# Kernel tuning notes

Hardware: AMD Instinct MI355X
Metric: run time of the kernel (lower is better)

## Reference

```python
import jax, jax.numpy as jnp
import numpy as np

B, T, I, H, V = 128, 80, 4096, 256, 6000
DEC_STEPS = 40


def _lstm_cell(x, h, c, Wih, Whh, b):
    # PyTorch gate order: i, f, g, o
    gates = x @ Wih.T + h @ Whh.T + b  # (B, 4H)
    i, f, g, o = jnp.split(gates, 4, axis=-1)
    c_new = jax.nn.sigmoid(f) * c + jax.nn.sigmoid(i) * jnp.tanh(g)
    h_new = jax.nn.sigmoid(o) * jnp.tanh(c_new)
    return h_new, c_new


def _lstm_scan(xs, h0, c0, Wih, Whh, b):
    # xs: (T, B, D)
    def step(carry, x):
        h, c = carry
        h, c = _lstm_cell(x, h, c, Wih, Whh, b)
        return (h, c), h
    (h, c), ys = jax.lax.scan(step, (h0, c0), xs)
    return ys, h, c


def setup_inputs() -> dict:
    key = jax.random.key(0)
    ks = jax.random.split(key, 11)
    s = 1.0 / np.sqrt(H)  # pytorch default LSTM init scale
    return {
        "x": jax.random.normal(ks[0], (B, T, I), jnp.float32),
        "W_ih1": jax.random.uniform(ks[1], (4 * H, I), jnp.float32, -s, s),
        "W_hh1": jax.random.uniform(ks[2], (4 * H, H), jnp.float32, -s, s),
        "b_ih1": jax.random.uniform(ks[3], (4 * H,), jnp.float32, -s, s),
        "b_hh1": jax.random.uniform(ks[4], (4 * H,), jnp.float32, -s, s),
        "W_ih2": jax.random.uniform(ks[5], (4 * H, H), jnp.float32, -s, s),
        "W_hh2": jax.random.uniform(ks[6], (4 * H, H), jnp.float32, -s, s),
        "b_ih2": jax.random.uniform(ks[7], (4 * H,), jnp.float32, -s, s),
        "b_ih2": jax.random.uniform(ks[7], (4 * H,), jnp.float32, -s, s),
        "b_hh2": jax.random.uniform(ks[8], (4 * H,), jnp.float32, -s, s),
        "W_out": jax.random.uniform(ks[9], (V, H), jnp.float32, -s, s),
        "b_out": jax.random.uniform(ks[10], (V,), jnp.float32, -s, s),
    }


def reference(x, W_ih1, W_hh1, b_ih1, b_hh1, W_ih2, W_hh2, b_ih2, b_hh2, W_out, b_out):
    batch = x.shape[0]
    b1 = b_ih1 + b_hh1
    b2 = b_ih2 + b_hh2
    z = jnp.zeros((batch, H), x.dtype)

    # --- Encoding: lstm1 over video features, lstm2 over lstm1 outputs ---
    xs = jnp.transpose(x, (1, 0, 2))  # (T, B, I)
    ys1, h1, c1 = _lstm_scan(xs, z, z, W_ih1, W_hh1, b1)
    _, h2, c2 = _lstm_scan(ys1, z, z, W_ih2, W_hh2, b2)

    # --- One extra lstm1 step with zero padding (as in the source) ---
    dec_pad = jnp.zeros((batch, I), x.dtype)
    h1, c1 = _lstm_cell(dec_pad, h1, c1, W_ih1, W_hh1, b1)
    y2 = jnp.zeros((batch, H), x.dtype)

    def dec_step(carry, _):
        h1, c1, h2, c2, y2 = carry
        h1, c1 = _lstm_cell(dec_pad, h1, c1, W_ih1, W_hh1, b1)
        h2, c2 = _lstm_cell(h1 + y2, h2, c2, W_ih2, W_hh2, b2)
        return (h1, c1, h2, c2, h2), h2

    _, ys = jax.lax.scan(dec_step, (h1, c1, h2, c2, y2), None, length=DEC_STEPS)  # (40, B, H)
    feats = jnp.transpose(ys, (1, 0, 2)).reshape(-1, H)  # (B*40, H)
    return feats @ W_out.T + b_out  # (B*40, V)
```

## Files before the change

### kernel.cpp

```cpp
#include <hip/hip_runtime.h>

#define NB 128
#define NT 80
#define NI 4096
#define NH 256
#define G4 1024
#define NV 6000
#define NVP 6016
#define NDEC 40

typedef unsigned short ushort_t;
typedef __attribute__((ext_vector_type(8))) short bf16x8;
typedef __attribute__((ext_vector_type(4))) float f32x4;

__device__ __forceinline__ unsigned short f2bf(float f) {
  unsigned int x = __float_as_uint(f);
  x += 0x7FFFu + ((x >> 16) & 1u);
  return (unsigned short)(x >> 16);
}
__device__ __forceinline__ float bf2f(ushort_t u) {
  return __uint_as_float(((unsigned)u) << 16);
}
__device__ __forceinline__ ushort4 pack4(float4 v) {
  return make_ushort4(f2bf(v.x), f2bf(v.y), f2bf(v.z), f2bf(v.w));
}
__device__ __forceinline__ float ftanh(float x) {
  float xc = fminf(fmaxf(x, -12.f), 12.f);
  float e = __expf(2.f * xc);
  return (e - 1.f) * __builtin_amdgcn_rcpf(e + 1.f);
}
__device__ __forceinline__ float fsig(float x) {
  return __builtin_amdgcn_rcpf(1.f + __expf(-x));
}


__global__ __launch_bounds__(256) void k_cast_x(const float* __restrict__ x,
                                                ushort_t* __restrict__ xb) {
  const int t = blockIdx.x, b = blockIdx.y;
  const float* src = x + ((size_t)b * NT + t) * NI;
  ushort_t* dst = xb + ((size_t)t * NB + b) * NI;
#pragma unroll
  for (int s = 0; s < 4; ++s) {
    int j = s * 1024 + threadIdx.x * 4;
    float4 v = *(const float4*)(src + j);
    *(ushort4*)(dst + j) = pack4(v);
  }
}

__global__ __launch_bounds__(256) void k_cast_pad(const float* __restrict__ s,
                                                  ushort_t* __restrict__ d,
                                                  int nsrc, int ndst) {
  int i = (blockIdx.x * 256 + threadIdx.x) * 4;
  if (i >= ndst) return;
  ushort4 o;
  if (i < nsrc) {
    float4 v = *(const float4*)(s + i);
    o = pack4(v);
  } else {
    o = make_ushort4(0, 0, 0, 0);
  }
  *(ushort4*)(d + i) = o;
}

__global__ __launch_bounds__(256) void k_addw_bf(const float* __restrict__ a,
                                                 const float* __restrict__ b,
                                                 ushort_t* __restrict__ o) {
  int i = (blockIdx.x * 256 + threadIdx.x) * 4;
  float4 va = *(const float4*)(a + i);
  float4 vb = *(const float4*)(b + i);
  va.x += vb.x; va.y += vb.y; va.z += vb.z; va.w += vb.w;
  *(ushort4*)(o + i) = pack4(va);
}

__global__ __launch_bounds__(256) void k_subh(ushort_t* __restrict__ H1,
                                              const ushort_t* __restrict__ h2) {
  int i = (blockIdx.x * 256 + threadIdx.x) * 4;
  ushort_t* p = H1 + (size_t)NB * NH + i;
  const ushort_t* q = h2 + i;
#pragma unroll
  for (int k = 0; k < 4; ++k) p[k] = f2bf(bf2f(p[k]) - bf2f(q[k]));
}


#define GLDS(gp, lp)                                                     \
  __builtin_amdgcn_global_load_lds(                                      \
      (const __attribute__((address_space(1))) unsigned int*)(gp),       \
      (__attribute__((address_space(3))) unsigned int*)(lp), 16, 0, 0)

__global__ __launch_bounds__(256) void k_gemm(
    const ushort_t* __restrict__ A, const ushort_t* __restrict__ Bm,
    float* __restrict__ C, const float* __restrict__ ba,
    const float* __restrict__ bb, int Nreal, int K, int ldc, int mtiles) {
  __shared__ __align__(16) ushort_t Als[128 * 32];
  __shared__ __align__(16) ushort_t Bls[128 * 32];
  const int bid = blockIdx.x;
  const int mt = bid % mtiles, nt = bid / mtiles;
  const size_t m0 = (size_t)mt * 128, n0 = (size_t)nt * 128;
  const int tid = threadIdx.x, wave = tid >> 6, lane = tid & 63;
  const int wm = (wave & 1) * 64, wn = (wave >> 1) * 64;
  const int srow = wave * 16 + (lane >> 2), skcol = (lane & 3) * 8;
  const int fr = lane & 15, kb = (lane >> 4) * 8;

  f32x4 acc[4][4];
#pragma unroll
  for (int i = 0; i < 4; ++i)
#pragma unroll
    for (int j = 0; j < 4; ++j) acc[i][j] = (f32x4){0.f, 0.f, 0.f, 0.f};

  for (int kk = 0; kk < K; kk += 32) {
    __syncthreads();
#pragma unroll
    for (int p = 0; p < 2; ++p) {
      GLDS(A + (m0 + p * 64 + srow) * K + kk + skcol,
           &Als[(p * 64 + wave * 16) * 32]);
      GLDS(Bm + (n0 + p * 64 + srow) * K + kk + skcol,
           &Bls[(p * 64 + wave * 16) * 32]);
    }
    __syncthreads();
    bf16x8 af[4], bfr[4];
#pragma unroll
    for (int i = 0; i < 4; ++i)
      af[i] = *(const bf16x8*)&Als[(wm + i * 16 + fr) * 32 + kb];
#pragma unroll
    for (int j = 0; j < 4; ++j)
      bfr[j] = *(const bf16x8*)&Bls[(wn + j * 16 + fr) * 32 + kb];
#pragma unroll
    for (int i = 0; i < 4; ++i)
#pragma unroll
      for (int j = 0; j < 4; ++j)
        acc[i][j] = __builtin_amdgcn_mfma_f32_16x16x32_bf16(af[i], bfr[j],
                                                            acc[i][j], 0, 0, 0);
  }
  const int cr4 = (lane >> 4) * 4, ccn = lane & 15;
#pragma unroll
  for (int j = 0; j < 4; ++j) {
    int n = (int)n0 + wn + j * 16 + ccn;
    if (n < Nreal) {
      float bv = (ba ? ba[n] : 0.f) + (bb ? bb[n] : 0.f);
#pragma unroll
      for (int i = 0; i < 4; ++i) {
#pragma unroll
        for (int r = 0; r < 4; ++r) {
          size_t m = m0 + wm + i * 16 + cr4 + r;
          C[m * (size_t)ldc + n] = acc[i][j][r] + bv;
        }
      }
    }
  }
}


struct ChainArgs {
  const float* gIn0; const float* gIn1; int n0; int tStart; int tEnd;
  const ushort_t* W0;
  const float* biasA; const float* biasB;
  ushort_t* traj0; ushort_t* traj1; int t1bmaj;
  ushort_t* hSt; float* cSt;
};

#define LOAD_WREGS(Wb)                                                        \
  _Pragma("unroll") for (int g = 0; g < 3; ++g)                               \
  _Pragma("unroll") for (int h = 0; h < 2; ++h)                               \
  _Pragma("unroll") for (int kb = 0; kb < 8; ++kb)                            \
      wr[g * 2 + h][kb] = *(const bf16x8*)((Wb) +                             \
          (size_t)(g * 256 + cbase + h * 16 + cn) * NH + kb * 32 + kgrp * 8);

#define PIN_W()                                                               \
  _Pragma("unroll") for (int g = 0; g < 6; ++g)                               \
  _Pragma("unroll") for (int kb = 0; kb < 8; ++kb)                            \
      asm volatile("" : "+a"(wr[g][kb]));

#define LOAD_WLDS(Wb)                                                         \
  _Pragma("unroll") for (int h = 0; h < 2; ++h)                               \
  _Pragma("unroll") for (int kb = 0; kb < 8; ++kb)                            \
      *(bf16x8*)&WL[wv * 8192 + h * 4096 + kb * 512 + cn * 32 + kgrp * 8] =   \
          *(const bf16x8*)((Wb) +                                             \
          (size_t)(768 + cbase + h * 16 + cn) * NH + kb * 32 + kgrp * 8);

__device__ __forceinline__ void run_chain(const ChainArgs a, int bg,
                                          ushort_t* WL,
                                          ushort_t (*hTz)[16 * 264]) {
  const int tid = threadIdx.x;
  const int wv = tid >> 6, lane = tid & 63;
  const int cn = lane & 15;
  const int kgrp = lane >> 4;
  const int cbase = wv * 32;
  const int rsel = kgrp & 1;

  bf16x8 wr[6][8];
  LOAD_WREGS(a.W0);
  PIN_W();
  LOAD_WLDS(a.W0);

  for (int i = tid; i < 2 * 16 * 264; i += 512) ((ushort_t*)hTz)[i] = 0;
  __syncthreads();
  float cs[8];
  if (a.tStart == 0) {
#pragma unroll
    for (int i = 0; i < 8; ++i) cs[i] = 0.f;
  } else {
    for (int i = tid; i < 8 * 256; i += 512) {
      int b = i >> 8, col = i & 255;
      hTz[0][b * 264 + col] = a.hSt[(size_t)(bg * 8 + b) * NH + col];
    }
#pragma unroll
    for (int h = 0; h < 2; ++h)
#pragma unroll
      for (int e = 0; e < 4; ++e)
        cs[h * 4 + e] =
            a.cSt[(size_t)(bg * 8 + rsel * 4 + e) * NH + cbase + h * 16 + cn];
  }
  __syncthreads();

  int cur = 0;
  for (int t = a.tStart; t < a.tEnd; ++t) {
    const ushort_t* hTc = &hTz[cur][0];
    ushort_t* hTn = &hTz[cur ^ 1][0];
    const float* gseg = (t < a.n0) ? a.gIn0 : a.gIn1;
    const int tt = (t < a.n0) ? t : t - a.n0;
#pragma unroll
    for (int h = 0; h < 2; ++h) {
      const int gcol = cbase + h * 16 + cn;
      float in_[4][4];
      if (gseg) {
        const float* base = gseg + (size_t)tt * (NB * G4);
#pragma unroll
        for (int g = 0; g < 4; ++g)
#pragma unroll
          for (int e = 0; e < 4; ++e)
            in_[g][e] = base[(size_t)(bg * 8 + rsel * 4 + e) * G4 + g * 256 + gcol];
      } else {
#pragma unroll
        for (int g = 0; g < 4; ++g) {
          float b = a.biasA[g * 256 + gcol] + a.biasB[g * 256 + gcol];
#pragma unroll
          for (int e = 0; e < 4; ++e) in_[g][e] = b;
        }
      }
      f32x4 acc[4];
#pragma unroll
      for (int g = 0; g < 4; ++g) acc[g] = (f32x4){0.f, 0.f, 0.f, 0.f};
#pragma unroll
      for (int kb = 0; kb < 8; ++kb) {
        bf16x8 af = *(const bf16x8*)&hTc[cn * 264 + kb * 32 + kgrp * 8];
        bf16x8 bo = *(const bf16x8*)&WL[wv * 8192 + h * 4096 + kb * 512 +
                                        cn * 32 + kgrp * 8];
        acc[0] = __builtin_amdgcn_mfma_f32_16x16x32_bf16(af, wr[0 + h][kb],
                                                         acc[0], 0, 0, 0);
        acc[1] = __builtin_amdgcn_mfma_f32_16x16x32_bf16(af, wr[2 + h][kb],
                                                         acc[1], 0, 0, 0);
        acc[2] = __builtin_amdgcn_mfma_f32_16x16x32_bf16(af, wr[4 + h][kb],
                                                         acc[2], 0, 0, 0);
        acc[3] = __builtin_amdgcn_mfma_f32_16x16x32_bf16(af, bo, acc[3], 0, 0, 0);
      }
#pragma unroll
      for (int e = 0; e < 4; ++e) {
        float a0 = acc[0][e] + in_[0][e];
        float a1 = acc[1][e] + in_[1][e];
        float a2 = acc[2][e] + in_[2][e];
        float a3 = acc[3][e] + in_[3][e];
        float ig = fsig(a0);
        float fg = fsig(a1);
        float gg = ftanh(a2);
        float og = fsig(a3);
        float cn_ = fg * cs[h * 4 + e] + ig * gg;
        cs[h * 4 + e] = cn_;
        float hn = og * ftanh(cn_);
        unsigned short hb = f2bf(hn);
        if (lane < 32) {
          const int b = (lane >> 4) * 4 + e;
          hTn[b * 264 + gcol] = hb;
          const int bglob = bg * 8 + b;
          if (t < a.n0) {
            if (a.traj0)
              a.traj0[(size_t)t * (NB * NH) + (size_t)bglob * NH + gcol] = hb;
          } else if (a.traj1) {
            size_t idx = a.t1bmaj
                ? ((size_t)bglob * NDEC + (t - a.n0)) * NH + gcol
                : (size_t)(t - a.n0) * (NB * NH) + (size_t)bglob * NH + gcol;
            a.traj1[idx] = hb;
          }
        }
      }
    }
    __syncthreads();
    cur ^= 1;
  }

  for (int i = tid; i < 8 * 256; i += 512) {
    int b = i >> 8, col = i & 255;
    a.hSt[(size_t)(bg * 8 + b) * NH + col] = hTz[cur][b * 264 + col];
  }
  if (lane < 32) {
#pragma unroll
    for (int h = 0; h < 2; ++h)
#pragma unroll
      for (int e = 0; e < 4; ++e)
        a.cSt[(size_t)(bg * 8 + (lane >> 4) * 4 + e) * NH + cbase + h * 16 + cn] =
            cs[h * 4 + e];
  }
}

__global__ __launch_bounds__(512, 1) void p_lstm16(ChainArgs a) {
  __shared__ __align__(16) ushort_t WL[8 * 8192];
  __shared__ __align__(16) ushort_t hTz[2][16 * 264];
  run_chain(a, blockIdx.x, WL, hTz);
}

__global__ __launch_bounds__(512, 1) void p_dual(ChainArgs a, ChainArgs b) {
  __shared__ __align__(16) ushort_t WL[8 * 8192];
  __shared__ __align__(16) ushort_t hTz[2][16 * 264];
  if (blockIdx.x < 16)
    run_chain(a, blockIdx.x, WL, hTz);
  else
    run_chain(b, blockIdx.x - 16, WL, hTz);
}


extern "C" void kernel_launch(void* const* d_in, const int* in_sizes, int n_in,
                              void* d_out, int out_size, void* d_ws,
                              size_t ws_size, hipStream_t stream) {
  const float* x = (const float*)d_in[0];
  const float* Wih1 = (const float*)d_in[1];
  const float* Whh1 = (const float*)d_in[2];
  const float* bih1 = (const float*)d_in[3];
  const float* bhh1 = (const float*)d_in[4];
  const float* Wih2 = (const float*)d_in[5];
  const float* Whh2 = (const float*)d_in[6];
  const float* bih2 = (const float*)d_in[7];
  const float* bhh2 = (const float*)d_in[8];
  const float* Wout = (const float*)d_in[9];
  const float* bout = (const float*)d_in[10];
  char* ws = (char*)d_ws;

  ushort_t* x_bf   = (ushort_t*)(ws + 0);
  float*    G2buf  = (float*)(ws + 0);
  float*    G3buf  = (float*)(ws + 41943040);
  float*    Gbuf   = (float*)(ws + 83886080);
  ushort_t* Wih1b  = (ushort_t*)(ws + 125829120);
  ushort_t* Wih2b  = (ushort_t*)(ws + 134217728);
  ushort_t* Woutb  = (ushort_t*)(ws + 134742016);
  ushort_t* Whh1b  = (ushort_t*)(ws + 137822208);
  ushort_t* Whh2b  = (ushort_t*)(ws + 138346496);
  ushort_t* ys1    = (ushort_t*)(ws + 138870784);
  ushort_t* H1dec  = (ushort_t*)(ws + 144113664);
  ushort_t* feats  = (ushort_t*)(ws + 146800640);
  ushort_t* Wsumb  = (ushort_t*)(ws + 149422080);
  ushort_t* h1St   = (ushort_t*)(ws + 149946368);
  float*    c1St   = (float*)(ws + 150011904);
  ushort_t* h2St   = (ushort_t*)(ws + 150142976);
  float*    c2St   = (float*)(ws + 150208512);

  k_cast_x<<<dim3(NT, NB), 256, 0, stream>>>(x, x_bf);
  k_cast_pad<<<4096, 256, 0, stream>>>(Wih1, Wih1b, G4 * NI, G4 * NI);
  k_cast_pad<<<256, 256, 0, stream>>>(Wih2, Wih2b, G4 * NH, G4 * NH);
  k_cast_pad<<<1504, 256, 0, stream>>>(Wout, Woutb, NV * NH, NVP * NH);
  k_cast_pad<<<256, 256, 0, stream>>>(Whh1, Whh1b, G4 * NH, G4 * NH);
  k_cast_pad<<<256, 256, 0, stream>>>(Whh2, Whh2b, G4 * NH, G4 * NH);
  k_addw_bf<<<256, 256, 0, stream>>>(Wih2, Whh2, Wsumb);

  k_gemm<<<640, 256, 0, stream>>>(x_bf, Wih1b, Gbuf, bih1, bhh1, G4, NI, G4, 80);

  ChainArgs c1{Gbuf, nullptr, NT, 0, 0, Whh1b,
               bih1, bhh1, ys1, H1dec, 0, h1St, c1St};
  ChainArgs c2{G2buf, G3buf, NT, 0, 0, Whh2b,
               bih2, bhh2, nullptr, feats, 1, h2St, c2St};

  ChainArgs e1a = c1; e1a.tStart = 0; e1a.tEnd = 40;
  p_lstm16<<<16, 512, 0, stream>>>(e1a);

  k_gemm<<<320, 256, 0, stream>>>(ys1, Wih2b, G2buf, bih2, bhh2, G4, NH, G4, 40);

  ChainArgs e1b = c1; e1b.tStart = 40; e1b.tEnd = 80;
  ChainArgs e2a = c2; e2a.tStart = 0; e2a.tEnd = 40;
  p_dual<<<32, 512, 0, stream>>>(e1b, e2a);

  k_gemm<<<320, 256, 0, stream>>>(ys1 + (size_t)40 * NB * NH, Wih2b,
                                  G2buf + (size_t)40 * NB * G4, bih2, bhh2,
                                  G4, NH, G4, 40);

  ChainArgs p1 = c1; p1.tStart = 80; p1.tEnd = 121;
  ChainArgs e2b = c2; e2b.tStart = 40; e2b.tEnd = 80;
  p_dual<<<32, 512, 0, stream>>>(p1, e2b);

  k_subh<<<32, 256, 0, stream>>>(H1dec, h2St);

  k_gemm<<<320, 256, 0, stream>>>(H1dec + (size_t)NB * NH, Wih2b, G3buf, bih2,
                                  bhh2, G4, NH, G4, 40);

  ChainArgs d2 = c2; d2.W0 = Wsumb; d2.tStart = 80; d2.tEnd = 120;
  p_lstm16<<<16, 512, 0, stream>>>(d2);

  k_gemm<<<40 * 47, 256, 0, stream>>>(feats, Woutb, (float*)d_out, bout, nullptr,
                                      NV, NH, NV, 40);
}
```

Before: 1.184 ms.

## Double recurrent LSTM block width to 16 waves, one column tile per wave

The recurrent LSTM kernels now launch 1024 threads (16 waves) per block instead of 512. Each wave owns 16 hidden columns instead of 32, which halves the register-resident recurrent weights per wave and drops the inner h loop. The h-state A fragments are also preloaded into registers before the MFMA loop. The aim is to shorten each serial timestep by spreading the per-step matmul and gate math over more waves, at the cost of a heavier block-wide barrier each step and the same 16-block grid.

```diff
diff --git a/kernel.cpp b/kernel.cpp
--- a/kernel.cpp
+++ b/kernel.cpp
@@ -160,22 +160,20 @@
 
 #define LOAD_WREGS(Wb)                                                        \
   _Pragma("unroll") for (int g = 0; g < 3; ++g)                               \
-  _Pragma("unroll") for (int h = 0; h < 2; ++h)                               \
   _Pragma("unroll") for (int kb = 0; kb < 8; ++kb)                            \
-      wr[g * 2 + h][kb] = *(const bf16x8*)((Wb) +                             \
-          (size_t)(g * 256 + cbase + h * 16 + cn) * NH + kb * 32 + kgrp * 8);
+      wr[g][kb] = *(const bf16x8*)((Wb) +                                     \
+          (size_t)(g * 256 + cbase + cn) * NH + kb * 32 + kgrp * 8);
 
 #define PIN_W()                                                               \
-  _Pragma("unroll") for (int g = 0; g < 6; ++g)                               \
+  _Pragma("unroll") for (int g = 0; g < 3; ++g)                               \
   _Pragma("unroll") for (int kb = 0; kb < 8; ++kb)                            \
       asm volatile("" : "+a"(wr[g][kb]));
 
 #define LOAD_WLDS(Wb)                                                         \
-  _Pragma("unroll") for (int h = 0; h < 2; ++h)                               \
   _Pragma("unroll") for (int kb = 0; kb < 8; ++kb)                            \
-      *(bf16x8*)&WL[wv * 8192 + h * 4096 + kb * 512 + cn * 32 + kgrp * 8] =   \
+      *(bf16x8*)&WL[wv * 4096 + kb * 512 + cn * 32 + kgrp * 8] =              \
           *(const bf16x8*)((Wb) +                                             \
-          (size_t)(768 + cbase + h * 16 + cn) * NH + kb * 32 + kgrp * 8);
+          (size_t)(768 + cbase + cn) * NH + kb * 32 + kgrp * 8);
 
 __device__ __forceinline__ void run_chain(const ChainArgs a, int bg,
                                           ushort_t* WL,
@@ -184,31 +182,28 @@
   const int wv = tid >> 6, lane = tid & 63;
   const int cn = lane & 15;
   const int kgrp = lane >> 4;
-  const int cbase = wv * 32;
+  const int cbase = wv * 16;
   const int rsel = kgrp & 1;
 
-  bf16x8 wr[6][8];
+  bf16x8 wr[3][8];
   LOAD_WREGS(a.W0);
   PIN_W();
   LOAD_WLDS(a.W0);
 
-  for (int i = tid; i < 2 * 16 * 264; i += 512) ((ushort_t*)hTz)[i] = 0;
+  for (int i = tid; i < 2 * 16 * 264; i += 1024) ((ushort_t*)hTz)[i] = 0;
   __syncthreads();
-  float cs[8];
+  float cs[4];
   if (a.tStart == 0) {
 #pragma unroll
-    for (int i = 0; i < 8; ++i) cs[i] = 0.f;
+    for (int i = 0; i < 4; ++i) cs[i] = 0.f;
   } else {
-    for (int i = tid; i < 8 * 256; i += 512) {
+    for (int i = tid; i < 8 * 256; i += 1024) {
       int b = i >> 8, col = i & 255;
       hTz[0][b * 264 + col] = a.hSt[(size_t)(bg * 8 + b) * NH + col];
     }
 #pragma unroll
-    for (int h = 0; h < 2; ++h)
-#pragma unroll
-      for (int e = 0; e < 4; ++e)
-        cs[h * 4 + e] =
-            a.cSt[(size_t)(bg * 8 + rsel * 4 + e) * NH + cbase + h * 16 + cn];
+    for (int e = 0; e < 4; ++e)
+      cs[e] = a.cSt[(size_t)(bg * 8 + rsel * 4 + e) * NH + cbase + cn];
   }
   __syncthreads();
 
@@ -218,97 +213,95 @@
     ushort_t* hTn = &hTz[cur ^ 1][0];
     const float* gseg = (t < a.n0) ? a.gIn0 : a.gIn1;
     const int tt = (t < a.n0) ? t : t - a.n0;
-#pragma unroll
-    for (int h = 0; h < 2; ++h) {
-      const int gcol = cbase + h * 16 + cn;
-      float in_[4][4];
-      if (gseg) {
-        const float* base = gseg + (size_t)tt * (NB * G4);
-#pragma unroll
-        for (int g = 0; g < 4; ++g)
-#pragma unroll
-          for (int e = 0; e < 4; ++e)
-            in_[g][e] = base[(size_t)(bg * 8 + rsel * 4 + e) * G4 + g * 256 + gcol];
-      } else {
-#pragma unroll
-        for (int g = 0; g < 4; ++g) {
-          float b = a.biasA[g * 256 + gcol] + a.biasB[g * 256 + gcol];
-#pragma unroll
-          for (int e = 0; e < 4; ++e) in_[g][e] = b;
+    const int gcol = cbase + cn;
+
+    float in_[4][4];
+    if (gseg) {
+      const float* base = gseg + (size_t)tt * (NB * G4);
+#pragma unroll
+      for (int g = 0; g < 4; ++g)
+#pragma unroll
+        for (int e = 0; e < 4; ++e)
+          in_[g][e] = base[(size_t)(bg * 8 + rsel * 4 + e) * G4 + g * 256 + gcol];
+    } else {
+#pragma unroll
+      for (int g = 0; g < 4; ++g) {
+        float b = a.biasA[g * 256 + gcol] + a.biasB[g * 256 + gcol];
+#pragma unroll
+        for (int e = 0; e < 4; ++e) in_[g][e] = b;
+      }
+    }
+    bf16x8 af[8];
+#pragma unroll
+    for (int kb = 0; kb < 8; ++kb)
+      af[kb] = *(const bf16x8*)&hTc[cn * 264 + kb * 32 + kgrp * 8];
+    f32x4 acc[4];
+#pragma unroll
+    for (int g = 0; g < 4; ++g) acc[g] = (f32x4){0.f, 0.f, 0.f, 0.f};
+#pragma unroll
+    for (int kb = 0; kb < 8; ++kb) {
+      bf16x8 bo = *(const bf16x8*)&WL[wv * 4096 + kb * 512 + cn * 32 + kgrp * 8];
+      acc[0] = __builtin_amdgcn_mfma_f32_16x16x32_bf16(af[kb], wr[0][kb],
+                                                       acc[0], 0, 0, 0);
+      acc[1] = __builtin_amdgcn_mfma_f32_16x16x32_bf16(af[kb], wr[1][kb],
+                                                       acc[1], 0, 0, 0);
+      acc[2] = __builtin_amdgcn_mfma_f32_16x16x32_bf16(af[kb], wr[2][kb],
+                                                       acc[2], 0, 0, 0);
+      acc[3] = __builtin_amdgcn_mfma_f32_16x16x32_bf16(af[kb], bo, acc[3],
+                                                       0, 0, 0);
+    }
+#pragma unroll
+    for (int e = 0; e < 4; ++e) {
+      float a0 = acc[0][e] + in_[0][e];
+      float a1 = acc[1][e] + in_[1][e];
+      float a2 = acc[2][e] + in_[2][e];
+      float a3 = acc[3][e] + in_[3][e];
+      float ig = fsig(a0);
+      float fg = fsig(a1);
+      float gg = ftanh(a2);
+      float og = fsig(a3);
+      float cn_ = fg * cs[e] + ig * gg;
+      cs[e] = cn_;
+      float hn = og * ftanh(cn_);
+      unsigned short hb = f2bf(hn);
+      if (lane < 32) {
+        const int b = (lane >> 4) * 4 + e;
+        hTn[b * 264 + gcol] = hb;
+        const int bglob = bg * 8 + b;
+        if (t < a.n0) {
+          if (a.traj0)
+            a.traj0[(size_t)t * (NB * NH) + (size_t)bglob * NH + gcol] = hb;
+        } else if (a.traj1) {
+          size_t idx = a.t1bmaj
+              ? ((size_t)bglob * NDEC + (t - a.n0)) * NH + gcol
+              : (size_t)(t - a.n0) * (NB * NH) + (size_t)bglob * NH + gcol;
+          a.traj1[idx] = hb;
         }
       }
-      f32x4 acc[4];
-#pragma unroll
-      for (int g = 0; g < 4; ++g) acc[g] = (f32x4){0.f, 0.f, 0.f, 0.f};
-#pragma unroll
-      for (int kb = 0; kb < 8; ++kb) {
-        bf16x8 af = *(const bf16x8*)&hTc[cn * 264 + kb * 32 + kgrp * 8];
-        bf16x8 bo = *(const bf16x8*)&WL[wv * 8192 + h * 4096 + kb * 512 +
-                                        cn * 32 + kgrp * 8];
-        acc[0] = __builtin_amdgcn_mfma_f32_16x16x32_bf16(af, wr[0 + h][kb],
-                                                         acc[0], 0, 0, 0);
-        acc[1] = __builtin_amdgcn_mfma_f32_16x16x32_bf16(af, wr[2 + h][kb],
-                                                         acc[1], 0, 0, 0);
-        acc[2] = __builtin_amdgcn_mfma_f32_16x16x32_bf16(af, wr[4 + h][kb],
-                                                         acc[2], 0, 0, 0);
-        acc[3] = __builtin_amdgcn_mfma_f32_16x16x32_bf16(af, bo, acc[3], 0, 0, 0);
-      }
-#pragma unroll
-      for (int e = 0; e < 4; ++e) {
-        float a0 = acc[0][e] + in_[0][e];
-        float a1 = acc[1][e] + in_[1][e];
-        float a2 = acc[2][e] + in_[2][e];
-        float a3 = acc[3][e] + in_[3][e];
-        float ig = fsig(a0);
-        float fg = fsig(a1);
-        float gg = ftanh(a2);
-        float og = fsig(a3);
-        float cn_ = fg * cs[h * 4 + e] + ig * gg;
-        cs[h * 4 + e] = cn_;
-        float hn = og * ftanh(cn_);
-        unsigned short hb = f2bf(hn);
-        if (lane < 32) {
-          const int b = (lane >> 4) * 4 + e;
-          hTn[b * 264 + gcol] = hb;
-          const int bglob = bg * 8 + b;
-          if (t < a.n0) {
-            if (a.traj0)
-              a.traj0[(size_t)t * (NB * NH) + (size_t)bglob * NH + gcol] = hb;
-          } else if (a.traj1) {
-            size_t idx = a.t1bmaj
-                ? ((size_t)bglob * NDEC + (t - a.n0)) * NH + gcol
-                : (size_t)(t - a.n0) * (NB * NH) + (size_t)bglob * NH + gcol;
-            a.traj1[idx] = hb;
-          }
-        }
-      }
     }
     __syncthreads();
     cur ^= 1;
   }
 
-  for (int i = tid; i < 8 * 256; i += 512) {
+  for (int i = tid; i < 8 * 256; i += 1024) {
     int b = i >> 8, col = i & 255;
     a.hSt[(size_t)(bg * 8 + b) * NH + col] = hTz[cur][b * 264 + col];
   }
   if (lane < 32) {
 #pragma unroll
-    for (int h = 0; h < 2; ++h)
-#pragma unroll
-      for (int e = 0; e < 4; ++e)
-        a.cSt[(size_t)(bg * 8 + (lane >> 4) * 4 + e) * NH + cbase + h * 16 + cn] =
-            cs[h * 4 + e];
-  }
-}
-
-__global__ __launch_bounds__(512, 1) void p_lstm16(ChainArgs a) {
-  __shared__ __align__(16) ushort_t WL[8 * 8192];
+    for (int e = 0; e < 4; ++e)
+      a.cSt[(size_t)(bg * 8 + (lane >> 4) * 4 + e) * NH + cbase + cn] = cs[e];
+  }
+}
+
+__global__ __launch_bounds__(1024, 1) void p_lstm16(ChainArgs a) {
+  __shared__ __align__(16) ushort_t WL[16 * 4096];
   __shared__ __align__(16) ushort_t hTz[2][16 * 264];
   run_chain(a, blockIdx.x, WL, hTz);
 }
 
-__global__ __launch_bounds__(512, 1) void p_dual(ChainArgs a, ChainArgs b) {
-  __shared__ __align__(16) ushort_t WL[8 * 8192];
+__global__ __launch_bounds__(1024, 1) void p_dual(ChainArgs a, ChainArgs b) {
+  __shared__ __align__(16) ushort_t WL[16 * 4096];
   __shared__ __align__(16) ushort_t hTz[2][16 * 264];
   if (blockIdx.x < 16)
     run_chain(a, blockIdx.x, WL, hTz);
@@ -367,13 +360,13 @@
                bih2, bhh2, nullptr, feats, 1, h2St, c2St};
 
   ChainArgs e1a = c1; e1a.tStart = 0; e1a.tEnd = 40;
-  p_lstm16<<<16, 512, 0, stream>>>(e1a);
+  p_lstm16<<<16, 1024, 0, stream>>>(e1a);
 
   k_gemm<<<320, 256, 0, stream>>>(ys1, Wih2b, G2buf, bih2, bhh2, G4, NH, G4, 40);
 
   ChainArgs e1b = c1; e1b.tStart = 40; e1b.tEnd = 80;
   ChainArgs e2a = c2; e2a.tStart = 0; e2a.tEnd = 40;
-  p_dual<<<32, 512, 0, stream>>>(e1b, e2a);
+  p_dual<<<32, 1024, 0, stream>>>(e1b, e2a);
 
   k_gemm<<<320, 256, 0, stream>>>(ys1 + (size_t)40 * NB * NH, Wih2b,
                                   G2buf + (size_t)40 * NB * G4, bih2, bhh2,
@@ -381,7 +374,7 @@
 
   ChainArgs p1 = c1; p1.tStart = 80; p1.tEnd = 121;
   ChainArgs e2b = c2; e2b.tStart = 40; e2b.tEnd = 80;
-  p_dual<<<32, 512, 0, stream>>>(p1, e2b);
+  p_dual<<<32, 1024, 0, stream>>>(p1, e2b);
 
   k_subh<<<32, 256, 0, stream>>>(H1dec, h2St);
 
@@ -389,7 +382,7 @@
                                   bhh2, G4, NH, G4, 40);
 
   ChainArgs d2 = c2; d2.W0 = Wsumb; d2.tStart = 80; d2.tEnd = 120;
-  p_lstm16<<<16, 512, 0, stream>>>(d2);
+  p_lstm16<<<16, 1024, 0, stream>>>(d2);
 
   k_gemm<<<40 * 47, 256, 0, stream>>>(feats, Woutb, (float*)d_out, bout, nullptr,
                                       NV, NH, NV, 40);
```

Result: slower. 1.744 ms (+47.4%).
